# Optimization experiments

Hardware: AMD Instinct MI355X
Metric: run time of the kernel (lower is better)

Reference implementation:

```python
import jax, jax.numpy as jnp
import numpy as np

N_HEAD = 16
N_FEAT = 1024
D_K = N_FEAT // N_HEAD


def setup_inputs() -> dict:
    key = jax.random.key(0)
    ks = jax.random.split(key, 11)
    B, T1, T2 = 2, 2048, 2048
    s = 0.02
    return {
        "query": jax.random.normal(ks[0], (B, T1, N_FEAT), jnp.float32),
        "key_": jax.random.normal(ks[1], (B, T2, N_FEAT), jnp.float32),
        "value": jax.random.normal(ks[2], (B, T2, N_FEAT), jnp.float32),
        "mask": jnp.ones((B, T1, T2), jnp.int32),
        "Wq": jax.random.normal(ks[3], (N_FEAT, N_FEAT), jnp.float32) * s,
        "bq": jnp.zeros((N_FEAT,), jnp.float32),
        "Wk": jax.random.normal(ks[4], (N_FEAT, N_FEAT), jnp.float32) * s,
        "bk": jnp.zeros((N_FEAT,), jnp.float32),
        "Wv": jax.random.normal(ks[5], (N_FEAT, N_FEAT), jnp.float32) * s,
        "bv": jnp.zeros((N_FEAT,), jnp.float32),
        "Wo": jax.random.normal(ks[6], (N_FEAT, N_FEAT), jnp.float32) * s,
        "bo": jnp.zeros((N_FEAT,), jnp.float32),
    }


def reference(query, key_, value, mask, Wq, bq, Wk, bk, Wv, bv, Wo, bo):
    B = query.shape[0]
    # project and split heads: (B, T, F) -> (B, H, T, d_k)
    def heads(x, W, b):
        y = x @ W + b
        return y.reshape(B, -1, N_HEAD, D_K).transpose(0, 2, 1, 3)

    q = heads(query, Wq, bq)
    k = heads(key_, Wk, bk)
    v = heads(value, Wv, bv)

    scale = jnp.sqrt(jnp.asarray(D_K, jnp.float32))
    scores = jnp.einsum("bhqd,bhkd->bhqk", q, k) / scale  # (B,H,T1,T2)
    m = mask[:, None, :, :]  # (B,1,T1,T2)
    scores = jnp.where(m > 0, scores, jnp.asarray(-10000.0, scores.dtype))
    attn = jax.nn.softmax(scores, axis=-1)
    # dropout_rate = 0.0 / inference -> identity
    x = jnp.einsum("bhqk,bhkd->bhqd", attn, v)
    x = x.transpose(0, 2, 1, 3).reshape(B, -1, N_FEAT)
    return x @ Wo + bo
```

## Files before the change

### kernel.cpp

```cpp
#include <hip/hip_runtime.h>
#include <hip/hip_bf16.h>
#include <stdint.h>

typedef float  f32x4 __attribute__((ext_vector_type(4)));
typedef short  s16x8 __attribute__((ext_vector_type(8)));
typedef short  s16x4 __attribute__((ext_vector_type(4)));
typedef int    i32x4 __attribute__((ext_vector_type(4)));

#define DI __device__ __forceinline__

constexpr int Bb = 2, Tt = 2048, Ff = 1024, Hh = 16, Dk = 64;
constexpr int Mm = Bb * Tt;
constexpr float LOG2E = 1.44269504088896340736f;

DI ushort f2bf(float f) {
  unsigned u = __float_as_uint(f);
  unsigned r = (u + 0x7fffu + ((u >> 16) & 1u)) >> 16;
  return (ushort)r;
}

DI int cvt_pk_bf16(float lo, float hi) {
  __hip_bfloat162 t = __float22bfloat162_rn(make_float2(lo, hi));
  int w;
  __builtin_memcpy(&w, &t, 4);
  return w;
}

DI s16x8 pack8(const float4& a, const float4& b) {
  i32x4 w;
  w[0] = cvt_pk_bf16(a.x, a.y); w[1] = cvt_pk_bf16(a.z, a.w);
  w[2] = cvt_pk_bf16(b.x, b.y); w[3] = cvt_pk_bf16(b.z, b.w);
  return __builtin_bit_cast(s16x8, w);
}

DI void gload16(const void* g, void* l) {
  __builtin_amdgcn_global_load_lds(
      (__attribute__((address_space(1))) void*)g,
      (__attribute__((address_space(3))) void*)l, 16, 0, 0);
}

DI void wait_vm4() { asm volatile("s_waitcnt vmcnt(4)" ::: "memory"); }
DI void wait_vm6() { asm volatile("s_waitcnt vmcnt(6)" ::: "memory"); }
DI void wait_vm0() { asm volatile("s_waitcnt vmcnt(0)" ::: "memory"); }
DI void wait_lgkm0() { asm volatile("s_waitcnt lgkmcnt(0)" ::: "memory"); }

__global__ __launch_bounds__(256) void prep_kernel(
    const float* __restrict__ W0, const float* __restrict__ W1,
    const float* __restrict__ W2, const float* __restrict__ W3,
    ushort* __restrict__ Wt0, ushort* __restrict__ Wt1,
    ushort* __restrict__ Wt2, ushort* __restrict__ Wt3,
    const int* __restrict__ mask, int* __restrict__ flags) {
  const int bid = blockIdx.x;
  const int t = threadIdx.x;
  if (bid < 1024) {
    const int z = bid >> 8, bx = bid & 15, by = (bid >> 4) & 15;
    const float* W; ushort* Wt;
    switch (z) {
      case 0: W = W0; Wt = Wt0; break;
      case 1: W = W1; Wt = Wt1; break;
      case 2: W = W2; Wt = Wt2; break;
      default: W = W3; Wt = Wt3; break;
    }
    __shared__ float tile[64][65];
    const int k0 = by * 64, n0 = bx * 64;
    const int r = t >> 4, c4 = (t & 15) * 4;
#pragma unroll
    for (int i = 0; i < 4; i++) {
      const int row = r + i * 16;
      const float4 v = *(const float4*)(W + (size_t)(k0 + row) * Ff + n0 + c4);
      tile[row][c4] = v.x; tile[row][c4 + 1] = v.y; tile[row][c4 + 2] = v.z; tile[row][c4 + 3] = v.w;
    }
    __syncthreads();
#pragma unroll
    for (int i = 0; i < 4; i++) {
      const int n = r + i * 16;
      s16x4 o;
#pragma unroll
      for (int j = 0; j < 4; j++) o[j] = (short)f2bf(tile[c4 + j][n]);
      *(s16x4*)(Wt + (size_t)(n0 + n) * Ff + k0 + c4) = o;
    }
  } else {
    const int mb = bid - 1024;
    const int kb = mb & 31, qb = (mb >> 5) & 31, bz = mb >> 10;
    __shared__ int s;
    if (t == 0) s = 1;
    __syncthreads();
    int ok = 1;
#pragma unroll
    for (int i = 0; i < 4; i++) {
      const int row = qb * 64 + (t >> 4) + i * 16;
      const int4 v = *(const int4*)(mask + ((size_t)bz * Tt + row) * Tt + kb * 64 + (t & 15) * 4);
      ok &= (v.x > 0) & (v.y > 0) & (v.z > 0) & (v.w > 0);
    }
    atomicAnd(&s, ok);
    __syncthreads();
    if (t == 0) flags[(bz * 32 + qb) * 32 + kb] = s;
  }
}

DI void gemm_core(const ushort* __restrict__ A, const ushort* __restrict__ Bt,
                  const float* __restrict__ bias, void* __restrict__ Cout, float scale, int mode,
                  int m0, int n0) {
  __shared__ ushort Ads[3][128 * 32];
  __shared__ ushort Bds[3][128 * 32];
  const int tid = threadIdx.x, lane = tid & 63, w = tid >> 6;
  const int wr = w >> 1, wc = w & 1;
  const int g = lane >> 4, ln = lane & 15;
  const int strow = tid >> 2;
  const int stc = (tid & 3) * 8;

  const ushort* Asrc0 = A + (size_t)(m0 + strow) * Ff + stc;
  const ushort* Asrc1 = A + (size_t)(m0 + 64 + strow) * Ff + stc;
  const ushort* Bsrc0 = Bt + (size_t)(n0 + strow) * Ff + stc;
  const ushort* Bsrc1 = Bt + (size_t)(n0 + 64 + strow) * Ff + stc;
  const int dst0 = strow * 32 + stc;
  const int dst1 = (64 + strow) * 32 + stc;

  f32x4 acc[4][4];
#pragma unroll
  for (int m = 0; m < 4; m++)
#pragma unroll
    for (int n = 0; n < 4; n++) acc[m][n] = (f32x4){0.f, 0.f, 0.f, 0.f};

  auto stage = [&](int t, int slot) {
    const int k0 = t * 32;
    gload16(Asrc0 + k0, Ads[slot] + dst0);
    gload16(Asrc1 + k0, Ads[slot] + dst1);
    gload16(Bsrc0 + k0, Bds[slot] + dst0);
    gload16(Bsrc1 + k0, Bds[slot] + dst1);
  };

  stage(0, 0);
  stage(1, 1);

  int rs = 0, ws = 2;
  for (int t = 0; t < 32; ++t) {
    if (t < 31) wait_vm4(); else wait_vm0();
    __builtin_amdgcn_s_barrier();
    __builtin_amdgcn_sched_barrier(0);
    if (t < 30) stage(t + 2, ws);
    const ushort* As = Ads[rs];
    const ushort* Bs = Bds[rs];
    s16x8 af[4], bf[4];
#pragma unroll
    for (int m = 0; m < 4; m++) af[m] = *(const s16x8*)(As + (wr * 64 + m * 16 + ln) * 32 + g * 8);
#pragma unroll
    for (int n = 0; n < 4; n++) bf[n] = *(const s16x8*)(Bs + (wc * 64 + n * 16 + ln) * 32 + g * 8);
    __builtin_amdgcn_s_setprio(1);
#pragma unroll
    for (int m = 0; m < 4; m++)
#pragma unroll
      for (int n = 0; n < 4; n++)
        acc[m][n] = __builtin_amdgcn_mfma_f32_16x16x32_bf16(af[m], bf[n], acc[m][n], 0, 0, 0);
    __builtin_amdgcn_s_setprio(0);
    rs = rs == 2 ? 0 : rs + 1;
    ws = ws == 2 ? 0 : ws + 1;
  }
#pragma unroll
  for (int m = 0; m < 4; m++) {
    const int r0 = m0 + wr * 64 + m * 16 + g * 4;
#pragma unroll
    for (int n = 0; n < 4; n++) {
      const int col = n0 + wc * 64 + n * 16 + ln;
      const float bv = bias[col];
#pragma unroll
      for (int r = 0; r < 4; r++) {
        const float val = (acc[m][n][r] + bv) * scale;
        if (mode == 1)
          ((ushort*)Cout)[(size_t)(r0 + r) * Ff + col] = f2bf(val);
        else
          ((float*)Cout)[(size_t)(r0 + r) * Ff + col] = val;
      }
    }
  }
}

DI void gemm_core_f32a(const float* __restrict__ A, const ushort* __restrict__ Bt,
                       const float* __restrict__ bias, void* __restrict__ Cout, float scale,
                       int mode, int m0, int n0) {
  __shared__ ushort Ads[3][128 * 32];
  __shared__ ushort Bds[3][128 * 32];
  const int tid = threadIdx.x, lane = tid & 63, w = tid >> 6;
  const int wr = w >> 1, wc = w & 1;
  const int g = lane >> 4, ln = lane & 15;
  const int strow = tid >> 2;
  const int stc = (tid & 3) * 8;

  const float*  Asrc0 = A + (size_t)(m0 + strow) * Ff + stc;
  const float*  Asrc1 = A + (size_t)(m0 + 64 + strow) * Ff + stc;
  const ushort* Bsrc0 = Bt + (size_t)(n0 + strow) * Ff + stc;
  const ushort* Bsrc1 = Bt + (size_t)(n0 + 64 + strow) * Ff + stc;
  const int dst0 = strow * 32 + stc;
  const int dst1 = (64 + strow) * 32 + stc;

  float4 rA0a, rA0b, rA1a, rA1b;
  auto loadA = [&](int t) {
    const float* p0 = Asrc0 + t * 32;
    const float* p1 = Asrc1 + t * 32;
    rA0a = *(const float4*)p0; rA0b = *(const float4*)(p0 + 4);
    rA1a = *(const float4*)p1; rA1b = *(const float4*)(p1 + 4);
  };
  auto writeA = [&](int slot) {
    *(s16x8*)(Ads[slot] + dst0) = pack8(rA0a, rA0b);
    *(s16x8*)(Ads[slot] + dst1) = pack8(rA1a, rA1b);
  };
  auto stageB = [&](int t, int slot) {
    const int k0 = t * 32;
    gload16(Bsrc0 + k0, Bds[slot] + dst0);
    gload16(Bsrc1 + k0, Bds[slot] + dst1);
  };

  f32x4 acc[4][4];
#pragma unroll
  for (int m = 0; m < 4; m++)
#pragma unroll
    for (int n = 0; n < 4; n++) acc[m][n] = (f32x4){0.f, 0.f, 0.f, 0.f};

  loadA(0);
  writeA(0);
  stageB(0, 0);
  loadA(1);
  stageB(1, 1);

  int rs = 0, ps = 1, ws = 2;
  for (int t = 0; t < 32; ++t) {
    if (t < 31) wait_vm6(); else wait_vm0();
    wait_lgkm0();
    __builtin_amdgcn_s_barrier();
    __builtin_amdgcn_sched_barrier(0);
    if (t < 31) writeA(ps);
    if (t < 30) { loadA(t + 2); stageB(t + 2, ws); }
    const ushort* As = Ads[rs];
    const ushort* Bs = Bds[rs];
    s16x8 af[4], bf[4];
#pragma unroll
    for (int m = 0; m < 4; m++) af[m] = *(const s16x8*)(As + (wr * 64 + m * 16 + ln) * 32 + g * 8);
#pragma unroll
    for (int n = 0; n < 4; n++) bf[n] = *(const s16x8*)(Bs + (wc * 64 + n * 16 + ln) * 32 + g * 8);
    __builtin_amdgcn_s_setprio(1);
#pragma unroll
    for (int m = 0; m < 4; m++)
#pragma unroll
      for (int n = 0; n < 4; n++)
        acc[m][n] = __builtin_amdgcn_mfma_f32_16x16x32_bf16(af[m], bf[n], acc[m][n], 0, 0, 0);
    __builtin_amdgcn_s_setprio(0);
    rs = rs == 2 ? 0 : rs + 1;
    ps = ps == 2 ? 0 : ps + 1;
    ws = ws == 2 ? 0 : ws + 1;
  }
#pragma unroll
  for (int m = 0; m < 4; m++) {
    const int r0 = m0 + wr * 64 + m * 16 + g * 4;
#pragma unroll
    for (int n = 0; n < 4; n++) {
      const int col = n0 + wc * 64 + n * 16 + ln;
      const float bv = bias[col];
      if (mode == 2) {
        const int bb = r0 >> 11, rb = r0 & 2047;
        const int x = rb & 63;
        const int pbase = (x & 0x20) | ((x & 0x0C) << 1) | ((x & 0x10) >> 2);
        s16x4 o4;
#pragma unroll
        for (int r = 0; r < 4; r++) o4[r] = (short)f2bf(acc[m][n][r] + bv);
        *(s16x4*)((ushort*)Cout + ((size_t)bb * Ff + col) * Tt + (rb & ~63) + pbase) = o4;
      } else {
#pragma unroll
        for (int r = 0; r < 4; r++)
          ((ushort*)Cout)[(size_t)(r0 + r) * Ff + col] = f2bf((acc[m][n][r] + bv) * scale);
      }
    }
  }
}

__global__ __launch_bounds__(256) void qkv_gemm_kernel(
    const float* __restrict__ Xq, const float* __restrict__ Xk, const float* __restrict__ Xv,
    const ushort* __restrict__ Wqt, const ushort* __restrict__ Wkt, const ushort* __restrict__ Wvt,
    const float* __restrict__ bq, const float* __restrict__ bk, const float* __restrict__ bv,
    ushort* __restrict__ Qb, ushort* __restrict__ Kb, ushort* __restrict__ Vpt) {
  const int lin = blockIdx.x + 8 * blockIdx.y + 256 * blockIdx.z;
  const int work = (lin & 7) * 96 + (lin >> 3);
  const int z = work >> 8;
  const int r = work & 255;
  const int m0 = (r >> 3) * 128, n0 = (r & 7) * 128;
  const float* A = z == 0 ? Xq : (z == 1 ? Xk : Xv);
  const ushort* Wt = z == 0 ? Wqt : (z == 1 ? Wkt : Wvt);
  const float* bias = z == 0 ? bq : (z == 1 ? bk : bv);
  void* C = z == 0 ? (void*)Qb : (z == 1 ? (void*)Kb : (void*)Vpt);
  const float scale = z == 0 ? 0.125f * LOG2E : 1.0f;
  gemm_core_f32a(A, Wt, bias, C, scale, z == 2 ? 2 : 1, m0, n0);
}

__global__ __launch_bounds__(256) void out_gemm_kernel(const ushort* __restrict__ AO,
                                                       const ushort* __restrict__ Wot,
                                                       const float* __restrict__ bo,
                                                       float* __restrict__ Out) {
  const int lin = blockIdx.x + 8 * blockIdx.y;
  const int work = (lin & 7) * 32 + (lin >> 3);
  const int m0 = (work >> 3) * 128, n0 = (work & 7) * 128;
  gemm_core(AO, Wot, bo, Out, 1.0f, 0, m0, n0);
}

__global__ __launch_bounds__(256) void flash_kernel(
    const ushort* __restrict__ Qb, const ushort* __restrict__ Kb, const ushort* __restrict__ Vpt,
    const int* __restrict__ flags, const int* __restrict__ mask, ushort* __restrict__ AO) {
  __shared__ ushort Ks[4][64 * 64];
  __shared__ ushort Vs[4][64 * 64];
  const int lin = blockIdx.x + 16 * (blockIdx.y + 16 * blockIdx.z);
  const int work = (lin & 7) * 64 + (lin >> 3);
  const int qb = work & 15, h = (work >> 4) & 15, b = work >> 8;
  const int tid = threadIdx.x, lane = tid & 63, w = tid >> 6;
  const int g = lane >> 4, ln = lane & 15;

  const ushort* Qg = Qb + ((size_t)b * Tt + qb * 128) * Ff + h * Dk;
  const ushort* Kg = Kb + ((size_t)b * Tt) * Ff + h * Dk;
  const ushort* Vg = Vpt + (size_t)(b * Ff + h * Dk) * Tt;

  const int srow = lane >> 3;
  const int swzch = ((lane & 7) ^ srow) * 8;

  const ushort* ksrc0 = Kg + (size_t)(w * 16 + srow) * Ff + swzch;
  const ushort* ksrc1 = ksrc0 + (size_t)8 * Ff;
  const ushort* vsrc0 = Vg + (size_t)(w * 16 + srow) * Tt + swzch;
  const ushort* vsrc1 = vsrc0 + (size_t)8 * Tt;

  s16x8 qf0[2], qf1[2];
  {
    const ushort* Qrow0 = Qg + (size_t)(w * 16 + ln) * Ff;
    const ushort* Qrow1 = Qrow0 + (size_t)64 * Ff;
    qf0[0] = *(const s16x8*)(Qrow0 + g * 8);
    qf0[1] = *(const s16x8*)(Qrow0 + 32 + g * 8);
    qf1[0] = *(const s16x8*)(Qrow1 + g * 8);
    qf1[1] = *(const s16x8*)(Qrow1 + 32 + g * 8);
  }
  const int* flagrow0 = flags + (b * 32 + qb * 2) * 32;
  const int f0 = (lane < 32) ? flagrow0[lane] : 1;
  const int f1 = (lane < 32) ? flagrow0[32 + lane] : 1;

  auto stage2 = [&](ushort* Kd0, ushort* Vd0, ushort* Kd1, ushort* Vd1) {
    const int r0 = w * 16;
    gload16(ksrc0, Kd0 + r0 * 64);
    gload16(ksrc1, Kd0 + (r0 + 8) * 64);
    gload16(vsrc0, Vd0 + r0 * 64);
    gload16(vsrc1, Vd0 + (r0 + 8) * 64);
    gload16(ksrc0 + (size_t)64 * Ff, Kd1 + r0 * 64);
    gload16(ksrc1 + (size_t)64 * Ff, Kd1 + (r0 + 8) * 64);
    gload16(vsrc0 + 64, Vd1 + r0 * 64);
    gload16(vsrc1 + 64, Vd1 + (r0 + 8) * 64);
    ksrc0 += (size_t)128 * Ff; ksrc1 += (size_t)128 * Ff;
    vsrc0 += 128; vsrc1 += 128;
  };

  stage2(Ks[0], Vs[0], Ks[1], Vs[1]);
  stage2(Ks[2], Vs[2], Ks[3], Vs[3]);
  __syncthreads();
  const unsigned long long bm0 = __ballot(f0 == 0);
  const unsigned long long bm1 = __ballot(f1 == 0);

  int loff[4][2];
#pragma unroll
  for (int i = 0; i < 4; i++)
#pragma unroll
    for (int c = 0; c < 2; c++) {
      const int row = i * 16 + ln;
      loff[i][c] = row * 128 + ((c * 64 + g * 16) ^ ((row & 7) << 4));
    }
  const char* Kbase = (const char*)&Ks[0][0];
  const char* Vbase = (const char*)&Vs[0][0];

  s16x8 onesf;
#pragma unroll
  for (int j = 0; j < 8; ++j) onesf[j] = (short)0x3F80;

  f32x4 accl0 = (f32x4){0.f, 0.f, 0.f, 0.f}, accl1 = (f32x4){0.f, 0.f, 0.f, 0.f};
  f32x4 o0[4], o1[4];
#pragma unroll
  for (int ds = 0; ds < 4; ds++) { o0[ds] = (f32x4){0.f, 0.f, 0.f, 0.f}; o1[ds] = (f32x4){0.f, 0.f, 0.f, 0.f}; }

  auto body = [&](int slot, int kt) {
    const char* Kc = Kbase + slot * 8192;
    const char* Vc = Vbase + slot * 8192;
    f32x4 sf0[4], sf1[4];
    __builtin_amdgcn_s_setprio(1);
#pragma unroll
    for (int ks = 0; ks < 4; ++ks) {
      f32x4 a0 = (f32x4){0.f, 0.f, 0.f, 0.f};
      f32x4 a1 = (f32x4){0.f, 0.f, 0.f, 0.f};
#pragma unroll
      for (int c = 0; c < 2; c++) {
        const s16x8 kf = *(const s16x8*)(Kc + loff[ks][c]);
        a0 = __builtin_amdgcn_mfma_f32_16x16x32_bf16(kf, qf0[c], a0, 0, 0, 0);
        a1 = __builtin_amdgcn_mfma_f32_16x16x32_bf16(kf, qf1[c], a1, 0, 0, 0);
      }
      sf0[ks] = a0; sf1[ks] = a1;
    }
    __builtin_amdgcn_s_setprio(0);
    if ((bm0 >> kt) & 1ull) {
      const int qg_ = qb * 128 + w * 16 + ln;
#pragma unroll
      for (int ks = 0; ks < 4; ++ks) {
        const int4 mv = *(const int4*)(mask + ((size_t)b * Tt + qg_) * Tt + kt * 64 + ks * 16 + g * 4);
        if (mv.x <= 0) sf0[ks][0] = -10000.f;
        if (mv.y <= 0) sf0[ks][1] = -10000.f;
        if (mv.z <= 0) sf0[ks][2] = -10000.f;
        if (mv.w <= 0) sf0[ks][3] = -10000.f;
      }
    }
    if ((bm1 >> kt) & 1ull) {
      const int qg_ = qb * 128 + 64 + w * 16 + ln;
#pragma unroll
      for (int ks = 0; ks < 4; ++ks) {
        const int4 mv = *(const int4*)(mask + ((size_t)b * Tt + qg_) * Tt + kt * 64 + ks * 16 + g * 4);
        if (mv.x <= 0) sf1[ks][0] = -10000.f;
        if (mv.y <= 0) sf1[ks][1] = -10000.f;
        if (mv.z <= 0) sf1[ks][2] = -10000.f;
        if (mv.w <= 0) sf1[ks][3] = -10000.f;
      }
    }
#pragma unroll
    for (int ks = 0; ks < 4; ++ks) {
#pragma unroll
      for (int r = 0; r < 4; ++r) {
        sf0[ks][r] = __builtin_amdgcn_exp2f(sf0[ks][r]);
        sf1[ks][r] = __builtin_amdgcn_exp2f(sf1[ks][r]);
      }
    }
    i32x4 paw0[2], paw1[2];
#pragma unroll
    for (int c = 0; c < 2; c++)
#pragma unroll
      for (int f = 0; f < 2; f++)
#pragma unroll
        for (int hh = 0; hh < 2; hh++) {
          paw0[c][f * 2 + hh] = cvt_pk_bf16(sf0[2 * c + f][2 * hh], sf0[2 * c + f][2 * hh + 1]);
          paw1[c][f * 2 + hh] = cvt_pk_bf16(sf1[2 * c + f][2 * hh], sf1[2 * c + f][2 * hh + 1]);
        }
    const s16x8 pa00 = __builtin_bit_cast(s16x8, paw0[0]);
    const s16x8 pa01 = __builtin_bit_cast(s16x8, paw0[1]);
    const s16x8 pa10 = __builtin_bit_cast(s16x8, paw1[0]);
    const s16x8 pa11 = __builtin_bit_cast(s16x8, paw1[1]);
    __builtin_amdgcn_s_setprio(1);
    accl0 = __builtin_amdgcn_mfma_f32_16x16x32_bf16(pa00, onesf, accl0, 0, 0, 0);
    accl0 = __builtin_amdgcn_mfma_f32_16x16x32_bf16(pa01, onesf, accl0, 0, 0, 0);
    accl1 = __builtin_amdgcn_mfma_f32_16x16x32_bf16(pa10, onesf, accl1, 0, 0, 0);
    accl1 = __builtin_amdgcn_mfma_f32_16x16x32_bf16(pa11, onesf, accl1, 0, 0, 0);
#pragma unroll
    for (int ds = 0; ds < 4; ++ds) {
#pragma unroll
      for (int c = 0; c < 2; ++c) {
        const s16x8 vf = *(const s16x8*)(Vc + loff[ds][c]);
        o0[ds] = __builtin_amdgcn_mfma_f32_16x16x32_bf16(c == 0 ? pa00 : pa01, vf, o0[ds], 0, 0, 0);
        o1[ds] = __builtin_amdgcn_mfma_f32_16x16x32_bf16(c == 0 ? pa10 : pa11, vf, o1[ds], 0, 0, 0);
      }
    }
    __builtin_amdgcn_s_setprio(0);
  };

  for (int kt = 0; kt < 32; kt += 4) {
    body(0, kt);
    body(1, kt + 1);
    __syncthreads();
    if (kt + 4 < 32) stage2(Ks[0], Vs[0], Ks[1], Vs[1]);
    body(2, kt + 2);
    body(3, kt + 3);
    __syncthreads();
    if (kt + 6 < 32) stage2(Ks[2], Vs[2], Ks[3], Vs[3]);
  }

  float inv0[4], inv1[4];
#pragma unroll
  for (int r = 0; r < 4; ++r) {
    inv0[r] = 1.0f / accl0[r];
    inv1[r] = 1.0f / accl1[r];
  }
  ushort* AOg0 = AO + ((size_t)b * Tt + qb * 128 + w * 16) * Ff + h * Dk;
  ushort* AOg1 = AOg0 + (size_t)64 * Ff;
#pragma unroll
  for (int ds = 0; ds < 4; ++ds)
#pragma unroll
    for (int r = 0; r < 4; ++r) {
      AOg0[(size_t)(g * 4 + r) * Ff + ds * 16 + ln] = f2bf(o0[ds][r] * inv0[r]);
      AOg1[(size_t)(g * 4 + r) * Ff + ds * 16 + ln] = f2bf(o1[ds][r] * inv1[r]);
    }
}

extern "C" void kernel_launch(void* const* d_in, const int* in_sizes, int n_in,
                              void* d_out, int out_size, void* d_ws, size_t ws_size,
                              hipStream_t stream) {
  const float* query = (const float*)d_in[0];
  const float* key_  = (const float*)d_in[1];
  const float* value = (const float*)d_in[2];
  const int*   mask  = (const int*)d_in[3];
  const float* Wq = (const float*)d_in[4];  const float* bq = (const float*)d_in[5];
  const float* Wk = (const float*)d_in[6];  const float* bk = (const float*)d_in[7];
  const float* Wv = (const float*)d_in[8];  const float* bv = (const float*)d_in[9];
  const float* Wo = (const float*)d_in[10]; const float* bo = (const float*)d_in[11];
  float* Out = (float*)d_out;

  constexpr size_t SZ_X = (size_t)Mm * Ff * 2;
  constexpr size_t SZ_W = (size_t)Ff * Ff * 2;
  uintptr_t p = (uintptr_t)d_ws;
  auto alloc = [&](size_t sz) { void* r = (void*)p; p += (sz + 255) & ~(size_t)255; return r; };
  ushort* AO  = (ushort*)alloc(SZ_X);
  ushort* Wqt = (ushort*)alloc(SZ_W);
  ushort* Wkt = (ushort*)alloc(SZ_W);
  ushort* Wvt = (ushort*)alloc(SZ_W);
  ushort* Wot = (ushort*)alloc(SZ_W);
  ushort* Qp  = (ushort*)alloc(SZ_X);
  ushort* Kp  = (ushort*)alloc(SZ_X);
  ushort* Vpt = (ushort*)alloc(SZ_X);
  int* flags = (int*)alloc((size_t)Bb * 32 * 32 * 4);

  prep_kernel<<<dim3(3072), 256, 0, stream>>>(Wq, Wk, Wv, Wo, Wqt, Wkt, Wvt, Wot, mask, flags);
  qkv_gemm_kernel<<<dim3(8, 32, 3), 256, 0, stream>>>(query, key_, value, Wqt, Wkt, Wvt,
                                                      bq, bk, bv, Qp, Kp, Vpt);
  flash_kernel<<<dim3(16, 16, 2), 256, 0, stream>>>(Qp, Kp, Vpt, flags, mask, AO);
  out_gemm_kernel<<<dim3(8, 32), 256, 0, stream>>>(AO, Wot, bo, Out);
}
```

Before: 124.8 us.

## Switch GEMM cores to BK=64 double-buffered LDS with XOR swizzle

Both projection GEMM cores move from a three-slot pipeline with K-step 32 and manual vmcnt waits to a two-slot double buffer with K-step 64, synchronised by __syncthreads. LDS tiles use an XOR swizzle on 16-byte chunks to avoid bank conflicts on the fragment reads. The aim is half as many barriers per tile, more MFMAs per barrier and fewer LDS conflicts. The cost is a shallower prefetch, which may expose global-load latency, plus more registers for the fp32 A staging.

```diff
diff --git a/kernel.cpp b/kernel.cpp
--- a/kernel.cpp
+++ b/kernel.cpp
@@ -38,11 +38,6 @@
       (__attribute__((address_space(1))) void*)g,
       (__attribute__((address_space(3))) void*)l, 16, 0, 0);
 }
-
-DI void wait_vm4() { asm volatile("s_waitcnt vmcnt(4)" ::: "memory"); }
-DI void wait_vm6() { asm volatile("s_waitcnt vmcnt(6)" ::: "memory"); }
-DI void wait_vm0() { asm volatile("s_waitcnt vmcnt(0)" ::: "memory"); }
-DI void wait_lgkm0() { asm volatile("s_waitcnt lgkmcnt(0)" ::: "memory"); }
 
 __global__ __launch_bounds__(256) void prep_kernel(
     const float* __restrict__ W0, const float* __restrict__ W1,
@@ -99,22 +94,14 @@
 }
 
 DI void gemm_core(const ushort* __restrict__ A, const ushort* __restrict__ Bt,
-                  const float* __restrict__ bias, void* __restrict__ Cout, float scale, int mode,
-                  int m0, int n0) {
-  __shared__ ushort Ads[3][128 * 32];
-  __shared__ ushort Bds[3][128 * 32];
+                  const float* __restrict__ bias, float* __restrict__ Cout, int m0, int n0) {
+  __shared__ ushort Ads[2][128 * 64];
+  __shared__ ushort Bds[2][128 * 64];
   const int tid = threadIdx.x, lane = tid & 63, w = tid >> 6;
   const int wr = w >> 1, wc = w & 1;
   const int g = lane >> 4, ln = lane & 15;
-  const int strow = tid >> 2;
-  const int stc = (tid & 3) * 8;
-
-  const ushort* Asrc0 = A + (size_t)(m0 + strow) * Ff + stc;
-  const ushort* Asrc1 = A + (size_t)(m0 + 64 + strow) * Ff + stc;
-  const ushort* Bsrc0 = Bt + (size_t)(n0 + strow) * Ff + stc;
-  const ushort* Bsrc1 = Bt + (size_t)(n0 + 64 + strow) * Ff + stc;
-  const int dst0 = strow * 32 + stc;
-  const int dst1 = (64 + strow) * 32 + stc;
+  const int srow = lane >> 3;
+  const int swzch = ((lane & 7) ^ srow) * 8;
 
   f32x4 acc[4][4];
 #pragma unroll
@@ -122,39 +109,49 @@
 #pragma unroll
     for (int n = 0; n < 4; n++) acc[m][n] = (f32x4){0.f, 0.f, 0.f, 0.f};
 
-  auto stage = [&](int t, int slot) {
-    const int k0 = t * 32;
-    gload16(Asrc0 + k0, Ads[slot] + dst0);
-    gload16(Asrc1 + k0, Ads[slot] + dst1);
-    gload16(Bsrc0 + k0, Bds[slot] + dst0);
-    gload16(Bsrc1 + k0, Bds[slot] + dst1);
+  auto stage = [&](int t, int buf) {
+    const int k0 = t * 64;
+#pragma unroll
+    for (int it = 0; it < 4; ++it) {
+      const int row = w * 32 + it * 8;
+      gload16(A + (size_t)(m0 + row + srow) * Ff + k0 + swzch, Ads[buf] + row * 64);
+      gload16(Bt + (size_t)(n0 + row + srow) * Ff + k0 + swzch, Bds[buf] + row * 64);
+    }
   };
 
   stage(0, 0);
-  stage(1, 1);
-
-  int rs = 0, ws = 2;
-  for (int t = 0; t < 32; ++t) {
-    if (t < 31) wait_vm4(); else wait_vm0();
-    __builtin_amdgcn_s_barrier();
-    __builtin_amdgcn_sched_barrier(0);
-    if (t < 30) stage(t + 2, ws);
-    const ushort* As = Ads[rs];
-    const ushort* Bs = Bds[rs];
-    s16x8 af[4], bf[4];
-#pragma unroll
-    for (int m = 0; m < 4; m++) af[m] = *(const s16x8*)(As + (wr * 64 + m * 16 + ln) * 32 + g * 8);
-#pragma unroll
-    for (int n = 0; n < 4; n++) bf[n] = *(const s16x8*)(Bs + (wc * 64 + n * 16 + ln) * 32 + g * 8);
+  __syncthreads();
+
+  for (int t = 0; t < 16; ++t) {
+    const int cur = t & 1;
+    if (t < 15) stage(t + 1, cur ^ 1);
+    s16x8 af[4][2], bf[4][2];
+#pragma unroll
+    for (int m = 0; m < 4; m++)
+#pragma unroll
+      for (int c = 0; c < 2; c++) {
+        const int ra = wr * 64 + m * 16 + ln;
+        const int off = (c * 64 + g * 16) ^ ((ra & 7) << 4);
+        af[m][c] = *(const s16x8*)((const char*)(Ads[cur]) + ra * 128 + off);
+      }
+#pragma unroll
+    for (int n = 0; n < 4; n++)
+#pragma unroll
+      for (int c = 0; c < 2; c++) {
+        const int rb = wc * 64 + n * 16 + ln;
+        const int off = (c * 64 + g * 16) ^ ((rb & 7) << 4);
+        bf[n][c] = *(const s16x8*)((const char*)(Bds[cur]) + rb * 128 + off);
+      }
     __builtin_amdgcn_s_setprio(1);
 #pragma unroll
     for (int m = 0; m < 4; m++)
 #pragma unroll
       for (int n = 0; n < 4; n++)
-        acc[m][n] = __builtin_amdgcn_mfma_f32_16x16x32_bf16(af[m], bf[n], acc[m][n], 0, 0, 0);
+#pragma unroll
+        for (int c = 0; c < 2; c++)
+          acc[m][n] = __builtin_amdgcn_mfma_f32_16x16x32_bf16(af[m][c], bf[n][c], acc[m][n], 0, 0, 0);
     __builtin_amdgcn_s_setprio(0);
-    rs = rs == 2 ? 0 : rs + 1;
-    ws = ws == 2 ? 0 : ws + 1;
+    if (t < 15) __syncthreads();
   }
 #pragma unroll
   for (int m = 0; m < 4; m++) {
@@ -164,13 +161,8 @@
       const int col = n0 + wc * 64 + n * 16 + ln;
       const float bv = bias[col];
 #pragma unroll
-      for (int r = 0; r < 4; r++) {
-        const float val = (acc[m][n][r] + bv) * scale;
-        if (mode == 1)
-          ((ushort*)Cout)[(size_t)(r0 + r) * Ff + col] = f2bf(val);
-        else
-          ((float*)Cout)[(size_t)(r0 + r) * Ff + col] = val;
-      }
+      for (int r = 0; r < 4; r++)
+        Cout[(size_t)(r0 + r) * Ff + col] = acc[m][n][r] + bv;
     }
   }
 }
@@ -178,36 +170,41 @@
 DI void gemm_core_f32a(const float* __restrict__ A, const ushort* __restrict__ Bt,
                        const float* __restrict__ bias, void* __restrict__ Cout, float scale,
                        int mode, int m0, int n0) {
-  __shared__ ushort Ads[3][128 * 32];
-  __shared__ ushort Bds[3][128 * 32];
+  __shared__ ushort Ads[2][128 * 64];
+  __shared__ ushort Bds[2][128 * 64];
   const int tid = threadIdx.x, lane = tid & 63, w = tid >> 6;
   const int wr = w >> 1, wc = w & 1;
   const int g = lane >> 4, ln = lane & 15;
-  const int strow = tid >> 2;
-  const int stc = (tid & 3) * 8;
-
-  const float*  Asrc0 = A + (size_t)(m0 + strow) * Ff + stc;
-  const float*  Asrc1 = A + (size_t)(m0 + 64 + strow) * Ff + stc;
-  const ushort* Bsrc0 = Bt + (size_t)(n0 + strow) * Ff + stc;
-  const ushort* Bsrc1 = Bt + (size_t)(n0 + 64 + strow) * Ff + stc;
-  const int dst0 = strow * 32 + stc;
-  const int dst1 = (64 + strow) * 32 + stc;
-
-  float4 rA0a, rA0b, rA1a, rA1b;
+  const int srow = lane >> 3;
+  const int swzch = ((lane & 7) ^ srow) * 8;
+
+  const int rwA = tid >> 1, ha = tid & 1;
+  const float* AsrcT = A + (size_t)(m0 + rwA) * Ff + ha * 32;
+  int awoff[4];
+#pragma unroll
+  for (int j = 0; j < 4; j++) {
+    const int ch = ha * 4 + j;
+    awoff[j] = rwA * 128 + ((ch * 16) ^ ((rwA & 7) << 4));
+  }
+
+  float4 rA[8];
   auto loadA = [&](int t) {
-    const float* p0 = Asrc0 + t * 32;
-    const float* p1 = Asrc1 + t * 32;
-    rA0a = *(const float4*)p0; rA0b = *(const float4*)(p0 + 4);
-    rA1a = *(const float4*)p1; rA1b = *(const float4*)(p1 + 4);
+    const float* p = AsrcT + t * 64;
+#pragma unroll
+    for (int j = 0; j < 8; j++) rA[j] = *(const float4*)(p + j * 4);
   };
-  auto writeA = [&](int slot) {
-    *(s16x8*)(Ads[slot] + dst0) = pack8(rA0a, rA0b);
-    *(s16x8*)(Ads[slot] + dst1) = pack8(rA1a, rA1b);
+  auto writeA = [&](int buf) {
+#pragma unroll
+    for (int j = 0; j < 4; j++)
+      *(s16x8*)((char*)(Ads[buf]) + awoff[j]) = pack8(rA[2 * j], rA[2 * j + 1]);
   };
-  auto stageB = [&](int t, int slot) {
-    const int k0 = t * 32;
-    gload16(Bsrc0 + k0, Bds[slot] + dst0);
-    gload16(Bsrc1 + k0, Bds[slot] + dst1);
+  auto stageB = [&](int t, int buf) {
+    const int k0 = t * 64;
+#pragma unroll
+    for (int it = 0; it < 4; ++it) {
+      const int row = w * 32 + it * 8;
+      gload16(Bt + (size_t)(n0 + row + srow) * Ff + k0 + swzch, Bds[buf] + row * 64);
+    }
   };
 
   f32x4 acc[4][4];
@@ -218,35 +215,42 @@
 
   loadA(0);
   writeA(0);
+  loadA(1);
   stageB(0, 0);
-  loadA(1);
-  stageB(1, 1);
-
-  int rs = 0, ps = 1, ws = 2;
-  for (int t = 0; t < 32; ++t) {
-    if (t < 31) wait_vm6(); else wait_vm0();
-    wait_lgkm0();
-    __builtin_amdgcn_s_barrier();
-    __builtin_amdgcn_sched_barrier(0);
-    if (t < 31) writeA(ps);
-    if (t < 30) { loadA(t + 2); stageB(t + 2, ws); }
-    const ushort* As = Ads[rs];
-    const ushort* Bs = Bds[rs];
-    s16x8 af[4], bf[4];
-#pragma unroll
-    for (int m = 0; m < 4; m++) af[m] = *(const s16x8*)(As + (wr * 64 + m * 16 + ln) * 32 + g * 8);
-#pragma unroll
-    for (int n = 0; n < 4; n++) bf[n] = *(const s16x8*)(Bs + (wc * 64 + n * 16 + ln) * 32 + g * 8);
+  __syncthreads();
+
+  for (int t = 0; t < 16; ++t) {
+    const int cur = t & 1;
+    if (t < 15) writeA(cur ^ 1);
+    if (t < 14) loadA(t + 2);
+    if (t < 15) stageB(t + 1, cur ^ 1);
+    s16x8 af[4][2], bf[4][2];
+#pragma unroll
+    for (int m = 0; m < 4; m++)
+#pragma unroll
+      for (int c = 0; c < 2; c++) {
+        const int ra = wr * 64 + m * 16 + ln;
+        const int off = (c * 64 + g * 16) ^ ((ra & 7) << 4);
+        af[m][c] = *(const s16x8*)((const char*)(Ads[cur]) + ra * 128 + off);
+      }
+#pragma unroll
+    for (int n = 0; n < 4; n++)
+#pragma unroll
+      for (int c = 0; c < 2; c++) {
+        const int rb = wc * 64 + n * 16 + ln;
+        const int off = (c * 64 + g * 16) ^ ((rb & 7) << 4);
+        bf[n][c] = *(const s16x8*)((const char*)(Bds[cur]) + rb * 128 + off);
+      }
     __builtin_amdgcn_s_setprio(1);
 #pragma unroll
     for (int m = 0; m < 4; m++)
 #pragma unroll
       for (int n = 0; n < 4; n++)
-        acc[m][n] = __builtin_amdgcn_mfma_f32_16x16x32_bf16(af[m], bf[n], acc[m][n], 0, 0, 0);
+#pragma unroll
+        for (int c = 0; c < 2; c++)
+          acc[m][n] = __builtin_amdgcn_mfma_f32_16x16x32_bf16(af[m][c], bf[n][c], acc[m][n], 0, 0, 0);
     __builtin_amdgcn_s_setprio(0);
-    rs = rs == 2 ? 0 : rs + 1;
-    ps = ps == 2 ? 0 : ps + 1;
-    ws = ws == 2 ? 0 : ws + 1;
+    if (t < 15) __syncthreads();
   }
 #pragma unroll
   for (int m = 0; m < 4; m++) {
@@ -297,7 +301,7 @@
   const int lin = blockIdx.x + 8 * blockIdx.y;
   const int work = (lin & 7) * 32 + (lin >> 3);
   const int m0 = (work >> 3) * 128, n0 = (work & 7) * 128;
-  gemm_core(AO, Wot, bo, Out, 1.0f, 0, m0, n0);
+  gemm_core(AO, Wot, bo, Out, m0, n0);
 }
 
 __global__ __launch_bounds__(256) void flash_kernel(
```

After: 162.1 us. +29.9%, slower.
